# Performance work log

Hardware: AMD Instinct MI355X
Metric: run time of the kernel (lower is better)

Reference implementation:

```python
import jax, jax.numpy as jnp
import numpy as np

BOUND = 1.0
NUM_STEPS = 128
MIN_NEAR = 0.05


def setup_inputs() -> dict:
    key = jax.random.key(0)
    ks = jax.random.split(key, 7)
    B, N, H = 2, 8192, 64
    # camera origins on a radius-2 sphere, rays aimed at jittered points near origin
    o = jax.random.normal(ks[0], (B, N, 3), jnp.float32)
    o = 2.0 * o / (jnp.linalg.norm(o, axis=-1, keepdims=True) + 1e-8)
    tgt = 0.5 * jax.random.normal(ks[1], (B, N, 3), jnp.float32)
    d = tgt - o
    d = d / (jnp.linalg.norm(d, axis=-1, keepdims=True) + 1e-8)
    W1 = jax.random.normal(ks[2], (3, H), jnp.float32) * 0.5
    W2 = jax.random.normal(ks[3], (3, H), jnp.float32) * 0.5
    b1 = jax.random.normal(ks[4], (H,), jnp.float32) * 0.1
    w_sigma = jax.random.normal(ks[5], (H, 1), jnp.float32) * 0.5
    W_color = jax.random.normal(ks[6], (H, 3), jnp.float32) * 0.5
    return {"rays_o": o, "rays_d": d, "W1": W1, "W2": W2, "b1": b1,
            "w_sigma": w_sigma, "W_color": W_color}


def _near_far(rays_o, rays_d):
    # cube AABB intersection (near_far_from_bound, type='cube')
    inv = 1.0 / (rays_d + 1e-15)
    tmin = (-BOUND - rays_o) * inv
    tmax = (BOUND - rays_o) * inv
    near = jnp.max(jnp.minimum(tmin, tmax), axis=-1, keepdims=True)  # [B,N,1]
    far = jnp.min(jnp.maximum(tmin, tmax), axis=-1, keepdims=True)
    miss = far < near
    near = jnp.where(miss, 1e9, near)
    far = jnp.where(miss, 1e9, far)
    near = jnp.maximum(near, MIN_NEAR)
    return near, far


def reference(rays_o, rays_d, W1, W2, b1, w_sigma, W_color):
    nears, fars = _near_far(rays_o, rays_d)                    # [B,N,1]
    t = jnp.linspace(0.0, 1.0, NUM_STEPS, dtype=jnp.float32)   # [S]
    z_vals = nears + (fars - nears) * t                        # [B,N,S]
    sample_dist = (fars - nears) / (NUM_STEPS - 1)             # [B,N,1]

    # sample points along rays, clamped to the AABB
    xyzs = rays_o[..., None, :] + rays_d[..., None, :] * z_vals[..., None]  # [B,N,S,3]
    xyzs = jnp.clip(xyzs, -BOUND, BOUND)

    # network stub: tiny per-sample MLP -> sigma [B,N,S], color [B,N,S,3]
    h = jax.nn.relu(jnp.einsum('bnsc,ch->bnsh', xyzs, W1)
                    + jnp.einsum('bnc,ch->bnh', rays_d, W2)[:, :, None, :]
                    + b1)
    sigma = jax.nn.softplus(jnp.einsum('bnsh,ho->bnso', h, w_sigma))[..., 0]
    rgbs = jax.nn.sigmoid(jnp.einsum('bnsh,hc->bnsc', h, W_color))

    # alpha compositing
    deltas = z_vals[..., 1:] - z_vals[..., :-1]                # [B,N,S-1]
    deltas = jnp.concatenate([deltas, sample_dist], axis=-1)   # [B,N,S]
    alphas = 1.0 - jnp.exp(-deltas * sigma)
    alphas_shifted = jnp.concatenate(
        [jnp.ones_like(alphas[..., :1]), 1.0 - alphas + 1e-15], axis=-1)
    weights = alphas * jnp.cumprod(alphas_shifted, axis=-1)[..., :-1]  # [B,N,S]

    weights_sum = weights.sum(axis=-1)                         # [B,N]
    depth = jnp.sum(weights * z_vals, axis=-1)                 # [B,N]
    image = jnp.sum(weights[..., None] * rgbs, axis=-2)        # [B,N,3], bg_color=0
    return image, depth, weights, weights_sum
```

## Files before the change

### kernel.cpp

```cpp
#include <hip/hip_runtime.h>
#include <math.h>

#define NSTEPS 128
#define HID 64
#define RAYS_PER_BLOCK 8
#define SAMPLES_PER_THREAD 4

__global__ __launch_bounds__(256, 6) void nerf_render_kernel(
    const float* __restrict__ rays_o,
    const float* __restrict__ rays_d,
    const float* __restrict__ W1,
    const float* __restrict__ W2,
    const float* __restrict__ b1,
    const float* __restrict__ w_sigma,
    const float* __restrict__ W_color,
    float* __restrict__ out_image,
    float* __restrict__ out_depth,
    float* __restrict__ out_weights,
    float* __restrict__ out_wsum,
    int R)
{
    const int tid = threadIdx.x;
    const int r   = tid >> 5;
    const int l   = tid & 31;
    int ray = blockIdx.x * RAYS_PER_BLOCK + r;
    const bool valid = (ray < R);
    if (!valid) ray = R - 1;

    const float o0 = rays_o[ray * 3 + 0];
    const float o1 = rays_o[ray * 3 + 1];
    const float o2 = rays_o[ray * 3 + 2];
    const float d0 = rays_d[ray * 3 + 0];
    const float d1 = rays_d[ray * 3 + 1];
    const float d2 = rays_d[ray * 3 + 2];

    const float inv0 = 1.0f / (d0 + 1e-15f);
    const float inv1 = 1.0f / (d1 + 1e-15f);
    const float inv2 = 1.0f / (d2 + 1e-15f);
    const float t0a = (-1.0f - o0) * inv0, t0b = (1.0f - o0) * inv0;
    const float t1a = (-1.0f - o1) * inv1, t1b = (1.0f - o1) * inv1;
    const float t2a = (-1.0f - o2) * inv2, t2b = (1.0f - o2) * inv2;
    float near = fmaxf(fmaxf(fminf(t0a, t0b), fminf(t1a, t1b)), fminf(t2a, t2b));
    float far  = fminf(fminf(fmaxf(t0a, t0b), fmaxf(t1a, t1b)), fmaxf(t2a, t2b));
    if (far < near) { near = 1e9f; far = 1e9f; }
    near = fmaxf(near, 0.05f);
    const float span = far - near;
    const float sample_dist = span * (1.0f / (NSTEPS - 1));

    float x0[SAMPLES_PER_THREAD], x1[SAMPLES_PER_THREAD], x2[SAMPLES_PER_THREAD];
#pragma unroll
    for (int k = 0; k < SAMPLES_PER_THREAD; k++) {
        const int s = l * SAMPLES_PER_THREAD + k;
        const float t = (float)s * (1.0f / (NSTEPS - 1));
        const float z = fmaf(span, t, near);
        x0[k] = fminf(fmaxf(fmaf(d0, z, o0), -1.0f), 1.0f);
        x1[k] = fminf(fmaxf(fmaf(d1, z, o1), -1.0f), 1.0f);
        x2[k] = fminf(fmaxf(fmaf(d2, z, o2), -1.0f), 1.0f);
    }

    float aS[SAMPLES_PER_THREAD] = {0.f, 0.f, 0.f, 0.f};
    float aR[SAMPLES_PER_THREAD] = {0.f, 0.f, 0.f, 0.f};
    float aG[SAMPLES_PER_THREAD] = {0.f, 0.f, 0.f, 0.f};
    float aB[SAMPLES_PER_THREAD] = {0.f, 0.f, 0.f, 0.f};

    for (int jc = 0; jc < HID; jc += 4) {
        const float4 w1x = *(const float4*)&W1[0 * HID + jc];
        const float4 w1y = *(const float4*)&W1[1 * HID + jc];
        const float4 w1z = *(const float4*)&W1[2 * HID + jc];
        const float4 w2x = *(const float4*)&W2[0 * HID + jc];
        const float4 w2y = *(const float4*)&W2[1 * HID + jc];
        const float4 w2z = *(const float4*)&W2[2 * HID + jc];
        const float4 bb  = *(const float4*)&b1[jc];
        const float4 ws  = *(const float4*)&w_sigma[jc];
        const float4 wc0 = *(const float4*)&W_color[jc * 3 + 0];
        const float4 wc1 = *(const float4*)&W_color[jc * 3 + 4];
        const float4 wc2 = *(const float4*)&W_color[jc * 3 + 8];

        const float c1x[4] = {w1x.x, w1x.y, w1x.z, w1x.w};
        const float c1y[4] = {w1y.x, w1y.y, w1y.z, w1y.w};
        const float c1z[4] = {w1z.x, w1z.y, w1z.z, w1z.w};
        const float c2x[4] = {w2x.x, w2x.y, w2x.z, w2x.w};
        const float c2y[4] = {w2y.x, w2y.y, w2y.z, w2y.w};
        const float c2z[4] = {w2z.x, w2z.y, w2z.z, w2z.w};
        const float cb[4]  = {bb.x, bb.y, bb.z, bb.w};
        const float cs[4]  = {ws.x, ws.y, ws.z, ws.w};
        const float ccr[4] = {wc0.x, wc0.w, wc1.z, wc2.y};
        const float ccg[4] = {wc0.y, wc1.x, wc1.w, wc2.z};
        const float ccb[4] = {wc0.z, wc1.y, wc2.x, wc2.w};

#pragma unroll
        for (int u = 0; u < 4; u++) {
            const float base = fmaf(d0, c2x[u], fmaf(d1, c2y[u], fmaf(d2, c2z[u], cb[u])));
#pragma unroll
            for (int k = 0; k < SAMPLES_PER_THREAD; k++) {
                float h = fmaf(x0[k], c1x[u], fmaf(x1[k], c1y[u], fmaf(x2[k], c1z[u], base)));
                h = fmaxf(h, 0.0f);
                aS[k] = fmaf(h, cs[u],  aS[k]);
                aR[k] = fmaf(h, ccr[u], aR[k]);
                aG[k] = fmaf(h, ccg[u], aG[k]);
                aB[k] = fmaf(h, ccb[u], aB[k]);
            }
        }
    }

    float alpha[SAMPLES_PER_THREAD], Tloc[SAMPLES_PER_THREAD];
    float pl = 1.0f;
#pragma unroll
    for (int k = 0; k < SAMPLES_PER_THREAD; k++) {
        const float x = aS[k];
        const float sig = fmaxf(x, 0.0f) + __logf(1.0f + __expf(-fabsf(x)));
        alpha[k] = 1.0f - __expf(-sample_dist * sig);
        Tloc[k] = pl;
        pl *= (1.0f - alpha[k] + 1e-15f);
    }

    float inc = pl;
#pragma unroll
    for (int dlt = 1; dlt < 32; dlt <<= 1) {
        const float v = __shfl_up(inc, dlt, 32);
        if (l >= dlt) inc *= v;
    }
    float excl = __shfl_up(inc, 1, 32);
    if (l == 0) excl = 1.0f;

    float w[SAMPLES_PER_THREAD];
    float wsum = 0.f, dep = 0.f, im0 = 0.f, im1 = 0.f, im2 = 0.f;
#pragma unroll
    for (int k = 0; k < SAMPLES_PER_THREAD; k++) {
        const int s = l * SAMPLES_PER_THREAD + k;
        const float t = (float)s * (1.0f / (NSTEPS - 1));
        const float z = fmaf(span, t, near);
        const float T  = excl * Tloc[k];
        const float wt = alpha[k] * T;
        w[k] = wt;
        wsum += wt;
        dep  += wt * z;
        const float cr = 1.0f / (1.0f + __expf(-aR[k]));
        const float cg = 1.0f / (1.0f + __expf(-aG[k]));
        const float cb2 = 1.0f / (1.0f + __expf(-aB[k]));
        im0 += wt * cr;
        im1 += wt * cg;
        im2 += wt * cb2;
    }

    if (valid) {
        *(float4*)&out_weights[(size_t)ray * NSTEPS + l * SAMPLES_PER_THREAD] =
            make_float4(w[0], w[1], w[2], w[3]);
    }

#pragma unroll
    for (int dlt = 16; dlt >= 1; dlt >>= 1) {
        wsum += __shfl_down(wsum, dlt, 32);
        dep  += __shfl_down(dep,  dlt, 32);
        im0  += __shfl_down(im0,  dlt, 32);
        im1  += __shfl_down(im1,  dlt, 32);
        im2  += __shfl_down(im2,  dlt, 32);
    }
    if (l == 0 && valid) {
        out_image[ray * 3 + 0] = im0;
        out_image[ray * 3 + 1] = im1;
        out_image[ray * 3 + 2] = im2;
        out_depth[ray] = dep;
        out_wsum[ray]  = wsum;
    }
}

extern "C" void kernel_launch(void* const* d_in, const int* in_sizes, int n_in,
                              void* d_out, int out_size, void* d_ws, size_t ws_size,
                              hipStream_t stream) {
    const float* rays_o  = (const float*)d_in[0];
    const float* rays_d  = (const float*)d_in[1];
    const float* W1      = (const float*)d_in[2];
    const float* W2      = (const float*)d_in[3];
    const float* b1      = (const float*)d_in[4];
    const float* w_sigma = (const float*)d_in[5];
    const float* W_color = (const float*)d_in[6];

    const int R = in_sizes[0] / 3;

    float* out         = (float*)d_out;
    float* out_image   = out;
    float* out_depth   = out_image + (size_t)R * 3;
    float* out_weights = out_depth + R;
    float* out_wsum    = out_weights + (size_t)R * NSTEPS;

    const int blocks = (R + RAYS_PER_BLOCK - 1) / RAYS_PER_BLOCK;
    nerf_render_kernel<<<blocks, 256, 0, stream>>>(
        rays_o, rays_d, W1, W2, b1, w_sigma, W_color,
        out_image, out_depth, out_weights, out_wsum, R);
}
```

Before: 97.40 us.

## Use packed fp16 FMA and dot2 for hidden layer with LDS-staged weights

Runs the per-sample MLP in packed half precision. Hidden-unit pairs are computed with two-wide fp16 FMAs, and the sigma and colour projections are accumulated with fdot2 into fp32. The per-ray direction bias and the packed weights are precomputed into shared memory once per block. Work is reshaped to 16 threads per ray with 8 samples each, and occupancy hints are adjusted to match. This cuts VALU instruction count roughly in half and removes redundant global weight loads, at the cost of fp16 rounding in the hidden activations.

```diff
diff --git a/kernel.cpp b/kernel.cpp
--- a/kernel.cpp
+++ b/kernel.cpp
@@ -3,10 +3,34 @@
 
 #define NSTEPS 128
 #define HID 64
-#define RAYS_PER_BLOCK 8
-#define SAMPLES_PER_THREAD 4
-
-__global__ __launch_bounds__(256, 6) void nerf_render_kernel(
+#define RAYS_PER_BLOCK 16
+#define THREADS_PER_RAY 16
+#define SPT 8
+
+typedef _Float16 hf2 __attribute__((ext_vector_type(2)));
+
+static __device__ __forceinline__ hf2 pk(float a, float b) {
+    auto v = __builtin_amdgcn_cvt_pkrtz(a, b);
+    return __builtin_bit_cast(hf2, v);
+}
+static __device__ __forceinline__ unsigned bits(hf2 v) {
+    return __builtin_bit_cast(unsigned, v);
+}
+static __device__ __forceinline__ hf2 unbits(unsigned u) {
+    return __builtin_bit_cast(hf2, u);
+}
+
+static __device__ __forceinline__ float dot2acc(hf2 h, hf2 w, float acc) {
+#if __has_builtin(__builtin_amdgcn_fdot2)
+    return __builtin_amdgcn_fdot2(h, w, acc, false);
+#else
+    acc = fmaf((float)h[0], (float)w[0], acc);
+    acc = fmaf((float)h[1], (float)w[1], acc);
+    return acc;
+#endif
+}
+
+__global__ __launch_bounds__(256, 4) void nerf_render_kernel(
     const float* __restrict__ rays_o,
     const float* __restrict__ rays_d,
     const float* __restrict__ W1,
@@ -20,9 +44,52 @@
     float* __restrict__ out_wsum,
     int R)
 {
+    __shared__ uint4 ldsA[RAYS_PER_BLOCK][33];
+    __shared__ uint4 ldsB[32];
+
     const int tid = threadIdx.x;
-    const int r   = tid >> 5;
-    const int l   = tid & 31;
+
+    for (int e = tid; e < RAYS_PER_BLOCK * 32; e += 256) {
+        const int r  = e >> 5;
+        const int jp = e & 31;
+        const int j0 = jp * 2;
+        int gray = blockIdx.x * RAYS_PER_BLOCK + r;
+        if (gray >= R) gray = R - 1;
+        const float dd0 = rays_d[gray * 3 + 0];
+        const float dd1 = rays_d[gray * 3 + 1];
+        const float dd2 = rays_d[gray * 3 + 2];
+        const float2 w1x = *(const float2*)&W1[0 * HID + j0];
+        const float2 w1y = *(const float2*)&W1[1 * HID + j0];
+        const float2 w1z = *(const float2*)&W1[2 * HID + j0];
+        const float2 w2x = *(const float2*)&W2[0 * HID + j0];
+        const float2 w2y = *(const float2*)&W2[1 * HID + j0];
+        const float2 w2z = *(const float2*)&W2[2 * HID + j0];
+        const float2 bb  = *(const float2*)&b1[j0];
+        const float bs0 = fmaf(dd0, w2x.x, fmaf(dd1, w2y.x, fmaf(dd2, w2z.x, bb.x)));
+        const float bs1 = fmaf(dd0, w2x.y, fmaf(dd1, w2y.y, fmaf(dd2, w2z.y, bb.y)));
+        uint4 v;
+        v.x = bits(pk(w1x.x, w1x.y));
+        v.y = bits(pk(w1y.x, w1y.y));
+        v.z = bits(pk(w1z.x, w1z.y));
+        v.w = bits(pk(bs0, bs1));
+        ldsA[r][jp] = v;
+    }
+    if (tid < 32) {
+        const int j0 = tid * 2;
+        const float2 ws = *(const float2*)&w_sigma[j0];
+        const float c00 = W_color[j0 * 3 + 0], c01 = W_color[j0 * 3 + 1], c02 = W_color[j0 * 3 + 2];
+        const float c10 = W_color[j0 * 3 + 3], c11 = W_color[j0 * 3 + 4], c12 = W_color[j0 * 3 + 5];
+        uint4 v;
+        v.x = bits(pk(ws.x, ws.y));
+        v.y = bits(pk(c00, c10));
+        v.z = bits(pk(c01, c11));
+        v.w = bits(pk(c02, c12));
+        ldsB[tid] = v;
+    }
+    __syncthreads();
+
+    const int r   = tid >> 4;
+    const int l   = tid & 15;
     int ray = blockIdx.x * RAYS_PER_BLOCK + r;
     const bool valid = (ray < R);
     if (!valid) ray = R - 1;
@@ -47,66 +114,55 @@
     const float span = far - near;
     const float sample_dist = span * (1.0f / (NSTEPS - 1));
 
-    float x0[SAMPLES_PER_THREAD], x1[SAMPLES_PER_THREAD], x2[SAMPLES_PER_THREAD];
-#pragma unroll
-    for (int k = 0; k < SAMPLES_PER_THREAD; k++) {
-        const int s = l * SAMPLES_PER_THREAD + k;
+    hf2 X0[SPT], X1[SPT], X2[SPT];
+#pragma unroll
+    for (int k = 0; k < SPT; k++) {
+        const int s = l * SPT + k;
         const float t = (float)s * (1.0f / (NSTEPS - 1));
         const float z = fmaf(span, t, near);
-        x0[k] = fminf(fmaxf(fmaf(d0, z, o0), -1.0f), 1.0f);
-        x1[k] = fminf(fmaxf(fmaf(d1, z, o1), -1.0f), 1.0f);
-        x2[k] = fminf(fmaxf(fmaf(d2, z, o2), -1.0f), 1.0f);
-    }
-
-    float aS[SAMPLES_PER_THREAD] = {0.f, 0.f, 0.f, 0.f};
-    float aR[SAMPLES_PER_THREAD] = {0.f, 0.f, 0.f, 0.f};
-    float aG[SAMPLES_PER_THREAD] = {0.f, 0.f, 0.f, 0.f};
-    float aB[SAMPLES_PER_THREAD] = {0.f, 0.f, 0.f, 0.f};
-
-    for (int jc = 0; jc < HID; jc += 4) {
-        const float4 w1x = *(const float4*)&W1[0 * HID + jc];
-        const float4 w1y = *(const float4*)&W1[1 * HID + jc];
-        const float4 w1z = *(const float4*)&W1[2 * HID + jc];
-        const float4 w2x = *(const float4*)&W2[0 * HID + jc];
-        const float4 w2y = *(const float4*)&W2[1 * HID + jc];
-        const float4 w2z = *(const float4*)&W2[2 * HID + jc];
-        const float4 bb  = *(const float4*)&b1[jc];
-        const float4 ws  = *(const float4*)&w_sigma[jc];
-        const float4 wc0 = *(const float4*)&W_color[jc * 3 + 0];
-        const float4 wc1 = *(const float4*)&W_color[jc * 3 + 4];
-        const float4 wc2 = *(const float4*)&W_color[jc * 3 + 8];
-
-        const float c1x[4] = {w1x.x, w1x.y, w1x.z, w1x.w};
-        const float c1y[4] = {w1y.x, w1y.y, w1y.z, w1y.w};
-        const float c1z[4] = {w1z.x, w1z.y, w1z.z, w1z.w};
-        const float c2x[4] = {w2x.x, w2x.y, w2x.z, w2x.w};
-        const float c2y[4] = {w2y.x, w2y.y, w2y.z, w2y.w};
-        const float c2z[4] = {w2z.x, w2z.y, w2z.z, w2z.w};
-        const float cb[4]  = {bb.x, bb.y, bb.z, bb.w};
-        const float cs[4]  = {ws.x, ws.y, ws.z, ws.w};
-        const float ccr[4] = {wc0.x, wc0.w, wc1.z, wc2.y};
-        const float ccg[4] = {wc0.y, wc1.x, wc1.w, wc2.z};
-        const float ccb[4] = {wc0.z, wc1.y, wc2.x, wc2.w};
-
-#pragma unroll
-        for (int u = 0; u < 4; u++) {
-            const float base = fmaf(d0, c2x[u], fmaf(d1, c2y[u], fmaf(d2, c2z[u], cb[u])));
-#pragma unroll
-            for (int k = 0; k < SAMPLES_PER_THREAD; k++) {
-                float h = fmaf(x0[k], c1x[u], fmaf(x1[k], c1y[u], fmaf(x2[k], c1z[u], base)));
-                h = fmaxf(h, 0.0f);
-                aS[k] = fmaf(h, cs[u],  aS[k]);
-                aR[k] = fmaf(h, ccr[u], aR[k]);
-                aG[k] = fmaf(h, ccg[u], aG[k]);
-                aB[k] = fmaf(h, ccb[u], aB[k]);
-            }
+        const float x0 = fminf(fmaxf(fmaf(d0, z, o0), -1.0f), 1.0f);
+        const float x1 = fminf(fmaxf(fmaf(d1, z, o1), -1.0f), 1.0f);
+        const float x2 = fminf(fmaxf(fmaf(d2, z, o2), -1.0f), 1.0f);
+        X0[k] = pk(x0, x0);
+        X1[k] = pk(x1, x1);
+        X2[k] = pk(x2, x2);
+    }
+
+    float aS[SPT] = {0,0,0,0,0,0,0,0};
+    float aR[SPT] = {0,0,0,0,0,0,0,0};
+    float aG[SPT] = {0,0,0,0,0,0,0,0};
+    float aB[SPT] = {0,0,0,0,0,0,0,0};
+    const hf2 zero2 = {(_Float16)0, (_Float16)0};
+
+#pragma unroll 2
+    for (int jp = 0; jp < 32; jp++) {
+        const uint4 A  = ldsA[r][jp];
+        const uint4 Bq = ldsB[jp];
+        const hf2 w1x = unbits(A.x);
+        const hf2 w1y = unbits(A.y);
+        const hf2 w1z = unbits(A.z);
+        const hf2 bse = unbits(A.w);
+        const hf2 wsg = unbits(Bq.x);
+        const hf2 wcr = unbits(Bq.y);
+        const hf2 wcg = unbits(Bq.z);
+        const hf2 wcb = unbits(Bq.w);
+#pragma unroll
+        for (int k = 0; k < SPT; k++) {
+            hf2 h = __builtin_elementwise_fma(X0[k], w1x,
+                    __builtin_elementwise_fma(X1[k], w1y,
+                    __builtin_elementwise_fma(X2[k], w1z, bse)));
+            h = __builtin_elementwise_max(h, zero2);
+            aS[k] = dot2acc(h, wsg, aS[k]);
+            aR[k] = dot2acc(h, wcr, aR[k]);
+            aG[k] = dot2acc(h, wcg, aG[k]);
+            aB[k] = dot2acc(h, wcb, aB[k]);
         }
     }
 
-    float alpha[SAMPLES_PER_THREAD], Tloc[SAMPLES_PER_THREAD];
+    float alpha[SPT], Tloc[SPT];
     float pl = 1.0f;
 #pragma unroll
-    for (int k = 0; k < SAMPLES_PER_THREAD; k++) {
+    for (int k = 0; k < SPT; k++) {
         const float x = aS[k];
         const float sig = fmaxf(x, 0.0f) + __logf(1.0f + __expf(-fabsf(x)));
         alpha[k] = 1.0f - __expf(-sample_dist * sig);
@@ -116,18 +172,18 @@
 
     float inc = pl;
 #pragma unroll
-    for (int dlt = 1; dlt < 32; dlt <<= 1) {
-        const float v = __shfl_up(inc, dlt, 32);
+    for (int dlt = 1; dlt < THREADS_PER_RAY; dlt <<= 1) {
+        const float v = __shfl_up(inc, dlt, THREADS_PER_RAY);
         if (l >= dlt) inc *= v;
     }
-    float excl = __shfl_up(inc, 1, 32);
+    float excl = __shfl_up(inc, 1, THREADS_PER_RAY);
     if (l == 0) excl = 1.0f;
 
-    float w[SAMPLES_PER_THREAD];
+    float w[SPT];
     float wsum = 0.f, dep = 0.f, im0 = 0.f, im1 = 0.f, im2 = 0.f;
 #pragma unroll
-    for (int k = 0; k < SAMPLES_PER_THREAD; k++) {
-        const int s = l * SAMPLES_PER_THREAD + k;
+    for (int k = 0; k < SPT; k++) {
+        const int s = l * SPT + k;
         const float t = (float)s * (1.0f / (NSTEPS - 1));
         const float z = fmaf(span, t, near);
         const float T  = excl * Tloc[k];
@@ -137,24 +193,25 @@
         dep  += wt * z;
         const float cr = 1.0f / (1.0f + __expf(-aR[k]));
         const float cg = 1.0f / (1.0f + __expf(-aG[k]));
-        const float cb2 = 1.0f / (1.0f + __expf(-aB[k]));
+        const float cb = 1.0f / (1.0f + __expf(-aB[k]));
         im0 += wt * cr;
         im1 += wt * cg;
-        im2 += wt * cb2;
+        im2 += wt * cb;
     }
 
     if (valid) {
-        *(float4*)&out_weights[(size_t)ray * NSTEPS + l * SAMPLES_PER_THREAD] =
-            make_float4(w[0], w[1], w[2], w[3]);
-    }
-
-#pragma unroll
-    for (int dlt = 16; dlt >= 1; dlt >>= 1) {
-        wsum += __shfl_down(wsum, dlt, 32);
-        dep  += __shfl_down(dep,  dlt, 32);
-        im0  += __shfl_down(im0,  dlt, 32);
-        im1  += __shfl_down(im1,  dlt, 32);
-        im2  += __shfl_down(im2,  dlt, 32);
+        float* wp = &out_weights[(size_t)ray * NSTEPS + l * SPT];
+        *(float4*)(wp + 0) = make_float4(w[0], w[1], w[2], w[3]);
+        *(float4*)(wp + 4) = make_float4(w[4], w[5], w[6], w[7]);
+    }
+
+#pragma unroll
+    for (int dlt = THREADS_PER_RAY / 2; dlt >= 1; dlt >>= 1) {
+        wsum += __shfl_down(wsum, dlt, THREADS_PER_RAY);
+        dep  += __shfl_down(dep,  dlt, THREADS_PER_RAY);
+        im0  += __shfl_down(im0,  dlt, THREADS_PER_RAY);
+        im1  += __shfl_down(im1,  dlt, THREADS_PER_RAY);
+        im2  += __shfl_down(im2,  dlt, THREADS_PER_RAY);
     }
     if (l == 0 && valid) {
         out_image[ray * 3 + 0] = im0;
```

New measurement: 90.37 us. 7.2% less time.
